# Optimization experiments

Hardware: AMD Instinct MI355X
Metric: run time of the kernel (lower is better)

The kernel has to match this reference:

```python
import jax, jax.numpy as jnp
import numpy as np

IN_C = 128
HIDE_C = 256
HC2 = HIDE_C // 2
OUT_C = 128
WS = 7          # winsize
SCALE = 0.125   # 1/8
EPS = 1e-5      # BatchNorm eps
B, H, W = 32, 112, 112


def setup_inputs() -> dict:
    key = jax.random.key(0)
    ks = jax.random.split(key, 24)
    f32 = jnp.float32

    def w(k, shape):
        return jax.random.normal(k, shape, f32) * 0.05

    def bn_params(k, c):
        k1, k2, k3, k4 = jax.random.split(k, 4)
        gamma = 1.0 + 0.1 * jax.random.normal(k1, (c,), f32)
        beta = 0.1 * jax.random.normal(k2, (c,), f32)
        mean = 0.1 * jax.random.normal(k3, (c,), f32)
        var = jax.random.uniform(k4, (c,), f32, 0.5, 1.5)
        return gamma, beta, mean, var

    x = jax.random.normal(ks[0], (B, IN_C, H, W), f32)
    wq = w(ks[1], (HC2, IN_C))
    gq, bq, mq, vq = bn_params(ks[2], HC2)
    wk = w(ks[3], (HC2, IN_C))
    gk, bk, mk, vk = bn_params(ks[4], HC2)
    wv = w(ks[5], (HIDE_C, IN_C))
    gv, bv, mv, vv = bn_params(ks[6], HIDE_C)
    wo = w(ks[7], (OUT_C, HIDE_C))
    bo = 0.05 * jax.random.normal(ks[8], (OUT_C,), f32)
    go, bbo, mo, vo = bn_params(ks[9], OUT_C)
    return {"x": x,
            "wq": wq, "gq": gq, "bq": bq, "mq": mq, "vq": vq,
            "wk": wk, "gk": gk, "bk": bk, "mk": mk, "vk": vk,
            "wv": wv, "gv": gv, "bv": bv, "mv": mv, "vv": vv,
            "wo": wo, "bo": bo, "go": go, "bbo": bbo, "mo": mo, "vo": vo}


def _conv1x1(x, w):
    # 1x1 conv, stride 1, no bias: pure channel contraction
    return jnp.einsum('bchw,oc->bohw', x, w)


def _bn(x, g, b, m, v):
    # inference-mode BatchNorm2d
    p = lambda a: a[None, :, None, None]
    return p(g) * (x - p(m)) * jax.lax.rsqrt(p(v) + EPS) + p(b)


def _to_windows(t):
    # 'b c (h1 ws1) (w1 ws2) -> b (c ws1 ws2) (h1 w1)'
    b, c, h, w = t.shape
    h1, w1 = h // WS, w // WS
    t = t.reshape(b, c, h1, WS, w1, WS).transpose(0, 1, 3, 5, 2, 4)
    return t.reshape(b, c * WS * WS, h1 * w1)


def _forward(x, wq, gq, bq, mq, vq, wk, gk, bk, mk, vk,
             wv, gv, bv, mv, vv, wo, bo, go, bbo, mo, vo):
    q = _bn(_conv1x1(x, wq), gq, bq, mq, vq)   # [B, HC2, H, W]
    k = _bn(_conv1x1(x, wk), gk, bk, mk, vk)   # [B, HC2, H, W]
    v = _bn(_conv1x1(x, wv), gv, bv, mv, vv)   # [B, HIDE_C, H, W]
    b, _, h, w = q.shape
    h1, w1 = h // WS, w // WS

    qf = _to_windows(q)  # [B, HC2*49, h1*w1]
    kf = _to_windows(k)
    vf = _to_windows(v)  # [B, HIDE_C*49, h1*w1]

    dots = jnp.einsum('bci,bcj->bij', qf, kf) * SCALE   # [B, T, T], T=h1*w1
    attn = jax.nn.softmax(dots, axis=-1)
    out = jnp.einsum('bij,bdj->bid', attn, vf)          # [B, T, HIDE_C*49]

    # 'b (h1 w1) (c1 ws1 ws2) -> b c1 (h1 ws1) (w1 ws2)'
    out = out.reshape(b, h1, w1, HIDE_C, WS, WS).transpose(0, 3, 1, 4, 2, 5)
    out = out.reshape(b, HIDE_C, h, w)

    out = jax.nn.gelu(out, approximate=False)
    out = _conv1x1(out, wo) + bo[None, :, None, None]
    out = _bn(out, go, bbo, mo, vo)
    # dropout is identity in eval; downsample is identity (stride=1, in_c==out_c)
    return jax.nn.gelu(out + x, approximate=False)


def reference(x, wq, gq, bq, mq, vq, wk, gk, bk, mk, vk,
              wv, gv, bv, mv, vv, wo, bo, go, bbo, mo, vo):
    return _forward(x, wq, gq, bq, mq, vq, wk, gk, bk, mk, vk,
                    wv, gv, bv, mv, vv, wo, bo, go, bbo, mo, vo)
```

## Files before the change

### kernel.cpp

```cpp
#include <hip/hip_runtime.h>


typedef unsigned short u16;
typedef unsigned int u32;
typedef short s16x8 __attribute__((ext_vector_type(8)));
typedef float f32x4 __attribute__((ext_vector_type(4)));
typedef u16 u16x8 __attribute__((ext_vector_type(8)));
typedef u16 u16x4 __attribute__((ext_vector_type(4)));

#define EPSV 1e-5f

__device__ __forceinline__ float bf2f(u16 h) {
  u32 u = ((u32)h) << 16;
  return __builtin_bit_cast(float, u);
}
__device__ __forceinline__ u16 f2bf(float f) {
  u32 u = __builtin_bit_cast(u32, f);
  u += 0x7FFFu + ((u >> 16) & 1u);
  return (u16)(u >> 16);
}
__device__ __forceinline__ s16x8 ld8(const u16* p) { return *(const s16x8*)p; }
__device__ __forceinline__ f32x4 mfma_bf16(s16x8 a, s16x8 b, f32x4 c) {
  return __builtin_amdgcn_mfma_f32_16x16x32_bf16(a, b, c, 0, 0, 0);
}
__device__ __forceinline__ float gelu_f(float v) {
  float e = exp2f(-2.3022083f * (v + 0.044715f * v * v * v));
  return v / (1.0f + e);
}

__global__ void k_params(
    const float* __restrict__ gq, const float* __restrict__ bq, const float* __restrict__ mq, const float* __restrict__ vq,
    const float* __restrict__ gk, const float* __restrict__ bk, const float* __restrict__ mk, const float* __restrict__ vk,
    const float* __restrict__ gv, const float* __restrict__ bv, const float* __restrict__ mv, const float* __restrict__ vv,
    const float* __restrict__ bo, const float* __restrict__ go, const float* __restrict__ bbo, const float* __restrict__ mo,
    const float* __restrict__ vo,
    float* __restrict__ sc512, float* __restrict__ sh512, float* __restrict__ sco, float* __restrict__ sho)
{
  const int i = threadIdx.x;
  if (i < 128) {
    const float s = gq[i] * rsqrtf(vq[i] + EPSV);
    sc512[i] = s;
    sh512[i] = bq[i] - mq[i] * s;
    const float so = go[i] * rsqrtf(vo[i] + EPSV);
    sco[i] = so;
    sho[i] = (bo[i] - mo[i]) * so + bbo[i];
  } else if (i < 256) {
    const int c = i - 128;
    const float s = gk[c] * rsqrtf(vk[c] + EPSV);
    sc512[i] = s;
    sh512[i] = bk[c] - mk[c] * s;
  } else if (i < 512) {
    const int c = i - 256;
    const float s = gv[c] * rsqrtf(vv[c] + EPSV);
    sc512[i] = s;
    sh512[i] = bv[c] - mv[c] * s;
  }
}

__global__ void k_wconv(const float* __restrict__ wq, const float* __restrict__ wk,
                        const float* __restrict__ wv, const float* __restrict__ sc512,
                        u16* __restrict__ wfused)
{
  const int idx4 = (blockIdx.x * 256 + threadIdx.x) * 4;
  const int co = idx4 >> 7, c = idx4 & 127;
  const float* src = (co < 128) ? (wq + co * 128 + c)
                   : (co < 256) ? (wk + (co - 128) * 128 + c)
                                : (wv + (co - 256) * 128 + c);
  const float s = sc512[co];
  const float4 v = *(const float4*)src;
  u16x4 r;
  r[0] = f2bf(v.x * s); r[1] = f2bf(v.y * s);
  r[2] = f2bf(v.z * s); r[3] = f2bf(v.w * s);
  *(u16x4*)(wfused + idx4) = r;
}

__global__ __launch_bounds__(256, 2) void k_qkv(
    const float* __restrict__ x, const u16* __restrict__ wfused,
    const float* __restrict__ sh512,
    u16* __restrict__ QW, u16* __restrict__ KW, u16* __restrict__ VW)
{
  __shared__ u16 XT[256 * 128];
  const int b = blockIdx.y;
  const int px0 = blockIdx.x * 256;
  const int t = threadIdx.x;

  {
    const float* xp = x + (size_t)b * 128u * 12544u + (size_t)(px0 + t);
    const int sw = (t & 15) << 3;
    #pragma unroll 8
    for (int c = 0; c < 128; c += 4) {
      u16x4 pk;
      pk[0] = f2bf(xp[(size_t)(c + 0) * 12544u]);
      pk[1] = f2bf(xp[(size_t)(c + 1) * 12544u]);
      pk[2] = f2bf(xp[(size_t)(c + 2) * 12544u]);
      pk[3] = f2bf(xp[(size_t)(c + 3) * 12544u]);
      *(u16x4*)&XT[t * 128 + (c ^ sw)] = pk;
    }
  }
  __syncthreads();

  const int w = t >> 6, l = t & 63, a15 = l & 15, g = l >> 4;

  s16x8 af[4][4];
  #pragma unroll
  for (int pxt = 0; pxt < 4; ++pxt) {
    const int row = w * 64 + pxt * 16 + a15;
    const int sw = (row & 15) << 3;
    #pragma unroll
    for (int ks = 0; ks < 4; ++ks) {
      const int cc = ks * 32 + g * 8;
      af[pxt][ks] = *(const s16x8*)&XT[row * 128 + (cc ^ sw)];
    }
  }
  __syncthreads();

  const int px = px0 + t;
  const int hh = px / 112, ww = px - hh * 112;
  const int h1 = hh / 7, p = hh - h1 * 7;
  const int w1 = ww / 7, q = ww - w1 * 7;
  const int j = h1 * 16 + w1, pq = p * 7 + q;
  u16* const qrow = QW + ((size_t)(b * 256 + j) * 49 + pq) * 128;
  u16* const krow = KW + ((size_t)(b * 256 + j) * 49 + pq) * 128;
  u16* const vrow = VW + (size_t)(b * 256 + j) * 12544 + pq * 256;

  #pragma unroll 1
  for (int phase = 0; phase < 4; ++phase) {
    s16x8 bcur[4];
    {
      const u16* wrow = wfused + (u32)(phase * 128 + a15) * 128u;
      #pragma unroll
      for (int ks = 0; ks < 4; ++ks) bcur[ks] = ld8(wrow + ks * 32 + g * 8);
    }
    #pragma unroll 1
    for (int cot8 = 0; cot8 < 8; ++cot8) {
      s16x8 bnext[4];
      if (cot8 < 7) {
        const u16* wrow = wfused + (u32)(phase * 128 + (cot8 + 1) * 16 + a15) * 128u;
        #pragma unroll
        for (int ks = 0; ks < 4; ++ks) bnext[ks] = ld8(wrow + ks * 32 + g * 8);
      }
      f32x4 acc[4];
      #pragma unroll
      for (int pxt = 0; pxt < 4; ++pxt) { acc[pxt][0]=0.f; acc[pxt][1]=0.f; acc[pxt][2]=0.f; acc[pxt][3]=0.f; }
      #pragma unroll
      for (int ks = 0; ks < 4; ++ks)
        #pragma unroll
        for (int pxt = 0; pxt < 4; ++pxt)
          acc[pxt] = mfma_bf16(af[pxt][ks], bcur[ks], acc[pxt]);

      const float sh = sh512[phase * 128 + cot8 * 16 + a15];
      const int co = cot8 * 16 + a15;
      #pragma unroll
      for (int pxt = 0; pxt < 4; ++pxt) {
        #pragma unroll
        for (int r = 0; r < 4; ++r) {
          const int pxl = w * 64 + pxt * 16 + g * 4 + r;
          XT[pxl * 128 + (co ^ ((pxl & 15) << 3))] = f2bf(acc[pxt][r] + sh);
        }
      }
      #pragma unroll
      for (int ks = 0; ks < 4; ++ks) bcur[ks] = bnext[ks];
    }
    __syncthreads();
    {
      u16* dst = (phase == 0) ? qrow : (phase == 1) ? krow : vrow + (phase - 2) * 128;
      const int sw = (t & 15) << 3;
      #pragma unroll
      for (int c8 = 0; c8 < 16; ++c8)
        *(u16x8*)(dst + c8 * 8) = *(const u16x8*)&XT[t * 128 + ((c8 * 8) ^ sw)];
    }
    __syncthreads();
  }
}

__global__ __launch_bounds__(512, 2) void k_dots(
    const u16* __restrict__ QW, const u16* __restrict__ KW, float* __restrict__ Pp)
{
  __shared__ u16 QS[256 * 64];
  __shared__ u16 KS[256 * 64];
  const int b = blockIdx.y, ks = blockIdx.x;
  const int nch = (ks == 7) ? 14 : 12;
  const int t = threadIdx.x;
  const int w = t >> 6, l = t & 63, a15 = l & 15, g = l >> 4;
  const int i0w = (w >> 1) * 64, j0w = (w & 1) * 128;

  f32x4 acc[4][8];
  #pragma unroll
  for (int i = 0; i < 4; ++i)
    #pragma unroll
    for (int j = 0; j < 8; ++j) { acc[i][j][0]=0.f; acc[i][j][1]=0.f; acc[i][j][2]=0.f; acc[i][j][3]=0.f; }

  const int srow = t >> 1;
  const int sgr0 = (t & 1) * 4;
  const size_t kb = (size_t)ks * 768 + (size_t)((t & 1) * 32);
  const u16* qsrc = QW + ((size_t)b * 256 + srow) * 6272 + kb;
  const u16* ksrc = KW + ((size_t)b * 256 + srow) * 6272 + kb;
  u16* qdst = &QS[srow * 64];
  u16* kdst = &KS[srow * 64];
  const int swr = srow & 7;

  for (int ch = 0; ch < nch; ++ch) {
    const int k0 = ch * 64;
    #pragma unroll
    for (int gi = 0; gi < 4; ++gi) {
      const int off = ((sgr0 + gi) ^ swr) << 3;
      *(u16x8*)(qdst + off) = *(const u16x8*)(qsrc + k0 + gi * 8);
      *(u16x8*)(kdst + off) = *(const u16x8*)(ksrc + k0 + gi * 8);
    }
    __syncthreads();
    #pragma unroll
    for (int kk = 0; kk < 2; ++kk) {
      s16x8 af[4], bfr[8];
      #pragma unroll
      for (int i4 = 0; i4 < 4; ++i4) {
        const int ir = i0w + i4 * 16 + a15;
        af[i4] = *(const s16x8*)&QS[ir * 64 + (((kk * 4 + g) ^ (ir & 7)) << 3)];
      }
      #pragma unroll
      for (int j8 = 0; j8 < 8; ++j8) {
        const int jr = j0w + j8 * 16 + a15;
        bfr[j8] = *(const s16x8*)&KS[jr * 64 + (((kk * 4 + g) ^ (jr & 7)) << 3)];
      }
      #pragma unroll
      for (int i4 = 0; i4 < 4; ++i4)
        #pragma unroll
        for (int j8 = 0; j8 < 8; ++j8)
          acc[i4][j8] = mfma_bf16(af[i4], bfr[j8], acc[i4][j8]);
    }
    __syncthreads();
  }

  float* pp = Pp + ((size_t)ks * 32 + b) * 256 * 256;
  #pragma unroll
  for (int i4 = 0; i4 < 4; ++i4)
    #pragma unroll
    for (int r = 0; r < 4; ++r) {
      const int ir = i0w + i4 * 16 + g * 4 + r;
      #pragma unroll
      for (int j8 = 0; j8 < 8; ++j8)
        pp[(size_t)ir * 256 + j0w + j8 * 16 + a15] = acc[i4][j8][r];
    }
}

__global__ __launch_bounds__(256, 4) void k_smax(const float* __restrict__ Pp, u16* __restrict__ P)
{
  const int b = blockIdx.y, it = blockIdx.x;
  const int t = threadIdx.x;
  const int row = it * 32 + (t >> 3);
  const int cg = t & 7;
  const size_t rb = ((size_t)b * 256 + row) * 256 + cg * 32;

  f32x4 s[8];
  #pragma unroll
  for (int cc = 0; cc < 8; ++cc) { s[cc][0]=0.f; s[cc][1]=0.f; s[cc][2]=0.f; s[cc][3]=0.f; }
  #pragma unroll 1
  for (int ks = 0; ks < 8; ++ks) {
    const float* src = Pp + (size_t)ks * 32 * 256 * 256 + rb;
    #pragma unroll
    for (int cc = 0; cc < 8; ++cc)
      s[cc] += *(const f32x4*)(src + cc * 4);
  }
  float m = -1e30f;
  #pragma unroll
  for (int cc = 0; cc < 8; ++cc)
    m = fmaxf(m, fmaxf(fmaxf(s[cc][0], s[cc][1]), fmaxf(s[cc][2], s[cc][3])));
  m = fmaxf(m, __shfl_xor(m, 1));
  m = fmaxf(m, __shfl_xor(m, 2));
  m = fmaxf(m, __shfl_xor(m, 4));
  const float CEXP = 0.18033688f;
  float sum = 0.f;
  #pragma unroll
  for (int cc = 0; cc < 8; ++cc)
    #pragma unroll
    for (int e = 0; e < 4; ++e) {
      const float p = exp2f((s[cc][e] - m) * CEXP);
      s[cc][e] = p;
      sum += p;
    }
  sum += __shfl_xor(sum, 1);
  sum += __shfl_xor(sum, 2);
  sum += __shfl_xor(sum, 4);
  const float inv = 1.0f / sum;
  u16* dst = P + rb;
  #pragma unroll
  for (int cc = 0; cc < 8; cc += 2) {
    u16x8 o;
    o[0] = f2bf(s[cc][0] * inv);     o[1] = f2bf(s[cc][1] * inv);
    o[2] = f2bf(s[cc][2] * inv);     o[3] = f2bf(s[cc][3] * inv);
    o[4] = f2bf(s[cc + 1][0] * inv); o[5] = f2bf(s[cc + 1][1] * inv);
    o[6] = f2bf(s[cc + 1][2] * inv); o[7] = f2bf(s[cc + 1][3] * inv);
    *(u16x8*)(dst + cc * 4) = o;
  }
}

__global__ __launch_bounds__(512, 2) void k_pv(
    const u16* __restrict__ P, const u16* __restrict__ VW, u16* __restrict__ GN)
{
  __shared__ u16 VT[256 * 64];
  __shared__ u16 PS[256 * 64];
  const int b = blockIdx.y, pq = blockIdx.x;
  const int t = threadIdx.x;
  const int w = t >> 6, l = t & 63, a15 = l & 15, g = l >> 4;
  const int m0w = (w >> 1) * 64, i0w = (w & 1) * 128;

  f32x4 acc[4][8];
  #pragma unroll
  for (int i = 0; i < 4; ++i)
    #pragma unroll
    for (int j = 0; j < 8; ++j) { acc[i][j][0]=0.f; acc[i][j][1]=0.f; acc[i][j][2]=0.f; acc[i][j][3]=0.f; }

  const int sj0 = (t & 7) * 8;
  const int sm0 = (t >> 3) * 4;
  const u16* vbase = VW + ((size_t)b * 256 + sj0) * 12544 + pq * 256 + sm0;
  const int prow = t >> 1;
  const int pgr0 = (t & 1) * 4;
  const u16* pbase = P + ((size_t)b * 256 + prow) * 256 + (t & 1) * 32;
  u16* psdst = &PS[prow * 64];
  const int pswr = prow & 7;

  for (int jc = 0; jc < 4; ++jc) {
    const int j0 = jc * 64;
    u16x4 rr[8];
    #pragma unroll
    for (int ji = 0; ji < 8; ++ji)
      rr[ji] = *(const u16x4*)(vbase + (size_t)(j0 + ji) * 12544);
    #pragma unroll
    for (int mi = 0; mi < 4; ++mi) {
      u16x8 wv;
      #pragma unroll
      for (int ji = 0; ji < 8; ++ji) wv[ji] = rr[ji][mi];
      const int m = sm0 + mi;
      *(u16x8*)&VT[m * 64 + (((sj0 >> 3) ^ (m & 7)) << 3)] = wv;
    }
    #pragma unroll
    for (int gi = 0; gi < 4; ++gi) {
      const int off = ((pgr0 + gi) ^ pswr) << 3;
      *(u16x8*)(psdst + off) = *(const u16x8*)(pbase + j0 + gi * 8);
    }
    __syncthreads();
    #pragma unroll
    for (int kk = 0; kk < 2; ++kk) {
      s16x8 av[4], bp[8];
      #pragma unroll
      for (int mf = 0; mf < 4; ++mf) {
        const int m = m0w + mf * 16 + a15;
        av[mf] = *(const s16x8*)&VT[m * 64 + (((kk * 4 + g) ^ (m & 7)) << 3)];
      }
      #pragma unroll
      for (int f = 0; f < 8; ++f) {
        const int i = i0w + f * 16 + a15;
        bp[f] = *(const s16x8*)&PS[i * 64 + (((kk * 4 + g) ^ (i & 7)) << 3)];
      }
      #pragma unroll
      for (int mf = 0; mf < 4; ++mf)
        #pragma unroll
        for (int f = 0; f < 8; ++f)
          acc[mf][f] = mfma_bf16(av[mf], bp[f], acc[mf][f]);
    }
    __syncthreads();
  }

  const int pp_ = pq / 7, qq = pq - 7 * pp_;
  #pragma unroll
  for (int f = 0; f < 8; ++f) {
    const int i = i0w + f * 16 + a15;
    const int h1 = i >> 4, w1 = i & 15;
    const size_t gb = ((size_t)b * 12544 + (size_t)((h1 * 7 + pp_) * 112 + w1 * 7 + qq)) * 256;
    #pragma unroll
    for (int mf = 0; mf < 4; ++mf) {
      u16x4 st;
      #pragma unroll
      for (int r = 0; r < 4; ++r) st[r] = f2bf(gelu_f(acc[mf][f][r]));
      *(u16x4*)&GN[gb + m0w + mf * 16 + g * 4] = st;
    }
  }
}

__global__ __launch_bounds__(512, 2) void k_out(
    const u16* __restrict__ GN, const float* __restrict__ wo,
    const float* __restrict__ x, const float* __restrict__ sco,
    const float* __restrict__ sho, float* __restrict__ out)
{
  __shared__ u16 WO[128 * 256];
  __shared__ u16 OT[128 * 264];
  const int b = blockIdx.y;
  const int px0 = blockIdx.x * 256;
  const int t = threadIdx.x;
  const int w = t >> 6, l = t & 63, a15 = l & 15, g = l >> 4;

  {
    const int o = t >> 2, gr0 = (t & 3) * 8;
    const float s = sco[o];
    const float* src = wo + o * 256 + gr0 * 8;
    u16* dr = &WO[o * 256];
    #pragma unroll
    for (int gi = 0; gi < 8; ++gi) {
      const float4 v0 = *(const float4*)(src + gi * 8);
      const float4 v1 = *(const float4*)(src + gi * 8 + 4);
      u16x8 pk;
      pk[0] = f2bf(v0.x * s); pk[1] = f2bf(v0.y * s);
      pk[2] = f2bf(v0.z * s); pk[3] = f2bf(v0.w * s);
      pk[4] = f2bf(v1.x * s); pk[5] = f2bf(v1.y * s);
      pk[6] = f2bf(v1.z * s); pk[7] = f2bf(v1.w * s);
      *(u16x8*)(dr + (((gr0 + gi) ^ (o & 7)) << 3)) = pk;
    }
  }
  __syncthreads();

  const int pw = w >> 1, ow = w & 1;
  const int o0w = ow * 64;
  f32x4 acc[4][4];
  #pragma unroll
  for (int i = 0; i < 4; ++i)
    #pragma unroll
    for (int j = 0; j < 4; ++j) { acc[i][j][0]=0.f; acc[i][j][1]=0.f; acc[i][j][2]=0.f; acc[i][j][3]=0.f; }

  #pragma unroll 1
  for (int ksl = 0; ksl < 8; ++ksl) {
    s16x8 af[4], bw[4];
    #pragma unroll
    for (int pxf = 0; pxf < 4; ++pxf) {
      const int row = px0 + pw * 64 + pxf * 16 + a15;
      af[pxf] = ld8(GN + ((size_t)b * 12544 + row) * 256 + ksl * 32 + g * 8);
    }
    #pragma unroll
    for (int of = 0; of < 4; ++of) {
      const int o = o0w + of * 16 + a15;
      bw[of] = *(const s16x8*)&WO[o * 256 + (((ksl * 4 + g) ^ (o & 7)) << 3)];
    }
    #pragma unroll
    for (int pxf = 0; pxf < 4; ++pxf)
      #pragma unroll
      for (int of = 0; of < 4; ++of)
        acc[pxf][of] = mfma_bf16(af[pxf], bw[of], acc[pxf][of]);
  }

  #pragma unroll
  for (int pxf = 0; pxf < 4; ++pxf)
    #pragma unroll
    for (int of = 0; of < 4; ++of) {
      u16x4 st;
      #pragma unroll
      for (int r = 0; r < 4; ++r) st[r] = f2bf(acc[pxf][of][r]);
      *(u16x4*)&OT[(o0w + of * 16 + a15) * 264 + pw * 64 + pxf * 16 + g * 4] = st;
    }
  __syncthreads();

  const int o2 = t >> 2;
  const float sh = sho[o2];
  const size_t xb = ((size_t)b * 128 + o2) * 12544 + px0;
  #pragma unroll 2
  for (int ii = 0; ii < 16; ++ii) {
    const int po = ii * 16 + (t & 3) * 4;
    const u16x4 zt = *(const u16x4*)&OT[o2 * 264 + po];
    const float4 xv = *(const float4*)(x + xb + po);
    float4 r;
    r.x = gelu_f(bf2f(zt[0]) + sh + xv.x);
    r.y = gelu_f(bf2f(zt[1]) + sh + xv.y);
    r.z = gelu_f(bf2f(zt[2]) + sh + xv.z);
    r.w = gelu_f(bf2f(zt[3]) + sh + xv.w);
    *(float4*)(out + xb + po) = r;
  }
}

extern "C" void kernel_launch(void* const* d_in, const int* in_sizes, int n_in,
                              void* d_out, int out_size, void* d_ws, size_t ws_size,
                              hipStream_t stream) {
  (void)in_sizes; (void)n_in; (void)out_size; (void)ws_size;
  const float* x   = (const float*)d_in[0];
  const float* wq  = (const float*)d_in[1];
  const float* gq  = (const float*)d_in[2];
  const float* bq  = (const float*)d_in[3];
  const float* mq  = (const float*)d_in[4];
  const float* vq  = (const float*)d_in[5];
  const float* wk  = (const float*)d_in[6];
  const float* gk  = (const float*)d_in[7];
  const float* bk  = (const float*)d_in[8];
  const float* mk  = (const float*)d_in[9];
  const float* vk  = (const float*)d_in[10];
  const float* wv  = (const float*)d_in[11];
  const float* gv  = (const float*)d_in[12];
  const float* bv  = (const float*)d_in[13];
  const float* mv  = (const float*)d_in[14];
  const float* vv  = (const float*)d_in[15];
  const float* wo  = (const float*)d_in[16];
  const float* bo  = (const float*)d_in[17];
  const float* go  = (const float*)d_in[18];
  const float* bbo = (const float*)d_in[19];
  const float* mo  = (const float*)d_in[20];
  const float* vo  = (const float*)d_in[21];

  u16* QW = (u16*)d_ws;
  u16* KW = QW + 51380224u;
  u16* VW = KW + 51380224u;
  u16* GN = VW + 102760448u;
  u16* P  = QW;
  float* Pp = (float*)GN;
  u16* wfused = GN;
  float* sc512 = (float*)(GN + 102760448u);
  float* sh512 = sc512 + 512;
  float* sco = sh512 + 512;
  float* sho = sco + 128;

  k_params<<<1, 512, 0, stream>>>(gq, bq, mq, vq, gk, bk, mk, vk, gv, bv, mv, vv,
                                  bo, go, bbo, mo, vo, sc512, sh512, sco, sho);
  k_wconv<<<64, 256, 0, stream>>>(wq, wk, wv, sc512, wfused);
  k_qkv<<<dim3(49, 32), 256, 0, stream>>>(x, wfused, sh512, QW, KW, VW);
  k_dots<<<dim3(8, 32), 512, 0, stream>>>(QW, KW, Pp);
  k_smax<<<dim3(8, 32), 256, 0, stream>>>(Pp, P);
  k_pv<<<dim3(49, 32), 512, 0, stream>>>(P, VW, GN);
  k_out<<<dim3(49, 32), 512, 0, stream>>>(GN, wo, x, sco, sho, (float*)d_out);
}
```

Baseline: 743.0 us.

## Precompute scaled bf16 output weights and retile qkv/out kernels for occupancy

Output-projection weights are now scaled and converted to bf16 once by a new kernel, in a workspace slot freed after the dots stage. The out kernel no longer stages them in LDS on every block and instead reads them from global/L2, using half-size pixel tiles with 256 threads to raise occupancy. k_qkv moves to 512 threads per block, with each wave handling 32 pixels and each thread half the channels, again to raise occupancy. The cost is extra global weight loads and one more kernel launch, and wof reuses KW memory, which relies on KW being dead by then.

```diff
diff --git a/kernel.cpp b/kernel.cpp
--- a/kernel.cpp
+++ b/kernel.cpp
@@ -74,7 +74,20 @@
   *(u16x4*)(wfused + idx4) = r;
 }
 
-__global__ __launch_bounds__(256, 2) void k_qkv(
+__global__ void k_woconv(const float* __restrict__ wo, const float* __restrict__ sco,
+                         u16* __restrict__ wof)
+{
+  const int idx4 = (blockIdx.x * 256 + threadIdx.x) * 4;
+  const int o = idx4 >> 8;
+  const float s = sco[o];
+  const float4 v = *(const float4*)(wo + idx4);
+  u16x4 r;
+  r[0] = f2bf(v.x * s); r[1] = f2bf(v.y * s);
+  r[2] = f2bf(v.z * s); r[3] = f2bf(v.w * s);
+  *(u16x4*)(wof + idx4) = r;
+}
+
+__global__ __launch_bounds__(512, 4) void k_qkv(
     const float* __restrict__ x, const u16* __restrict__ wfused,
     const float* __restrict__ sh512,
     u16* __restrict__ QW, u16* __restrict__ KW, u16* __restrict__ VW)
@@ -85,43 +98,45 @@
   const int t = threadIdx.x;
 
   {
-    const float* xp = x + (size_t)b * 128u * 12544u + (size_t)(px0 + t);
-    const int sw = (t & 15) << 3;
-    #pragma unroll 8
-    for (int c = 0; c < 128; c += 4) {
+    const int pxl = t & 255, cb = (t >> 8) * 64;
+    const float* xp = x + (size_t)b * 128u * 12544u + (size_t)cb * 12544u + (size_t)(px0 + pxl);
+    const int sw = (pxl & 15) << 3;
+    #pragma unroll 4
+    for (int i = 0; i < 16; ++i) {
+      const int c = i * 4;
       u16x4 pk;
       pk[0] = f2bf(xp[(size_t)(c + 0) * 12544u]);
       pk[1] = f2bf(xp[(size_t)(c + 1) * 12544u]);
       pk[2] = f2bf(xp[(size_t)(c + 2) * 12544u]);
       pk[3] = f2bf(xp[(size_t)(c + 3) * 12544u]);
-      *(u16x4*)&XT[t * 128 + (c ^ sw)] = pk;
+      *(u16x4*)&XT[pxl * 128 + ((cb + c) ^ sw)] = pk;
     }
   }
   __syncthreads();
 
   const int w = t >> 6, l = t & 63, a15 = l & 15, g = l >> 4;
 
-  s16x8 af[4][4];
-  #pragma unroll
-  for (int pxt = 0; pxt < 4; ++pxt) {
-    const int row = w * 64 + pxt * 16 + a15;
+  s16x8 af[2][4];
+  #pragma unroll
+  for (int pxt = 0; pxt < 2; ++pxt) {
+    const int row = w * 32 + pxt * 16 + a15;
     const int sw = (row & 15) << 3;
     #pragma unroll
-    for (int ks = 0; ks < 4; ++ks) {
-      const int cc = ks * 32 + g * 8;
-      af[pxt][ks] = *(const s16x8*)&XT[row * 128 + (cc ^ sw)];
-    }
+    for (int ks = 0; ks < 4; ++ks)
+      af[pxt][ks] = *(const s16x8*)&XT[row * 128 + ((ks * 32 + g * 8) ^ sw)];
   }
   __syncthreads();
 
-  const int px = px0 + t;
+  const int pxl = t & 255, chalf = (t >> 8) * 64;
+  const int px = px0 + pxl;
   const int hh = px / 112, ww = px - hh * 112;
   const int h1 = hh / 7, p = hh - h1 * 7;
   const int w1 = ww / 7, q = ww - w1 * 7;
   const int j = h1 * 16 + w1, pq = p * 7 + q;
-  u16* const qrow = QW + ((size_t)(b * 256 + j) * 49 + pq) * 128;
-  u16* const krow = KW + ((size_t)(b * 256 + j) * 49 + pq) * 128;
-  u16* const vrow = VW + (size_t)(b * 256 + j) * 12544 + pq * 256;
+  u16* const qrow = QW + ((size_t)(b * 256 + j) * 49 + pq) * 128 + chalf;
+  u16* const krow = KW + ((size_t)(b * 256 + j) * 49 + pq) * 128 + chalf;
+  u16* const vrow = VW + (size_t)(b * 256 + j) * 12544 + pq * 256 + chalf;
+  const int swf = (pxl & 15) << 3;
 
   #pragma unroll 1
   for (int phase = 0; phase < 4; ++phase) {
@@ -139,23 +154,23 @@
         #pragma unroll
         for (int ks = 0; ks < 4; ++ks) bnext[ks] = ld8(wrow + ks * 32 + g * 8);
       }
-      f32x4 acc[4];
-      #pragma unroll
-      for (int pxt = 0; pxt < 4; ++pxt) { acc[pxt][0]=0.f; acc[pxt][1]=0.f; acc[pxt][2]=0.f; acc[pxt][3]=0.f; }
+      f32x4 acc[2];
+      #pragma unroll
+      for (int pxt = 0; pxt < 2; ++pxt) { acc[pxt][0]=0.f; acc[pxt][1]=0.f; acc[pxt][2]=0.f; acc[pxt][3]=0.f; }
       #pragma unroll
       for (int ks = 0; ks < 4; ++ks)
         #pragma unroll
-        for (int pxt = 0; pxt < 4; ++pxt)
+        for (int pxt = 0; pxt < 2; ++pxt)
           acc[pxt] = mfma_bf16(af[pxt][ks], bcur[ks], acc[pxt]);
 
       const float sh = sh512[phase * 128 + cot8 * 16 + a15];
       const int co = cot8 * 16 + a15;
       #pragma unroll
-      for (int pxt = 0; pxt < 4; ++pxt) {
+      for (int pxt = 0; pxt < 2; ++pxt) {
         #pragma unroll
         for (int r = 0; r < 4; ++r) {
-          const int pxl = w * 64 + pxt * 16 + g * 4 + r;
-          XT[pxl * 128 + (co ^ ((pxl & 15) << 3))] = f2bf(acc[pxt][r] + sh);
+          const int prow = w * 32 + pxt * 16 + g * 4 + r;
+          XT[prow * 128 + (co ^ ((prow & 15) << 3))] = f2bf(acc[pxt][r] + sh);
         }
       }
       #pragma unroll
@@ -164,10 +179,9 @@
     __syncthreads();
     {
       u16* dst = (phase == 0) ? qrow : (phase == 1) ? krow : vrow + (phase - 2) * 128;
-      const int sw = (t & 15) << 3;
-      #pragma unroll
-      for (int c8 = 0; c8 < 16; ++c8)
-        *(u16x8*)(dst + c8 * 8) = *(const u16x8*)&XT[t * 128 + ((c8 * 8) ^ sw)];
+      #pragma unroll
+      for (int c8 = 0; c8 < 8; ++c8)
+        *(u16x8*)(dst + c8 * 8) = *(const u16x8*)&XT[pxl * 128 + ((chalf + c8 * 8) ^ swf)];
     }
     __syncthreads();
   }
@@ -376,39 +390,17 @@
   }
 }
 
-__global__ __launch_bounds__(512, 2) void k_out(
-    const u16* __restrict__ GN, const float* __restrict__ wo,
-    const float* __restrict__ x, const float* __restrict__ sco,
-    const float* __restrict__ sho, float* __restrict__ out)
-{
-  __shared__ u16 WO[128 * 256];
-  __shared__ u16 OT[128 * 264];
+__global__ __launch_bounds__(256, 3) void k_out(
+    const u16* __restrict__ GN, const u16* __restrict__ wof,
+    const float* __restrict__ x, const float* __restrict__ sho, float* __restrict__ out)
+{
+  __shared__ u16 OT[128 * 140];
   const int b = blockIdx.y;
-  const int px0 = blockIdx.x * 256;
+  const int px0 = blockIdx.x * 128;
   const int t = threadIdx.x;
   const int w = t >> 6, l = t & 63, a15 = l & 15, g = l >> 4;
-
-  {
-    const int o = t >> 2, gr0 = (t & 3) * 8;
-    const float s = sco[o];
-    const float* src = wo + o * 256 + gr0 * 8;
-    u16* dr = &WO[o * 256];
-    #pragma unroll
-    for (int gi = 0; gi < 8; ++gi) {
-      const float4 v0 = *(const float4*)(src + gi * 8);
-      const float4 v1 = *(const float4*)(src + gi * 8 + 4);
-      u16x8 pk;
-      pk[0] = f2bf(v0.x * s); pk[1] = f2bf(v0.y * s);
-      pk[2] = f2bf(v0.z * s); pk[3] = f2bf(v0.w * s);
-      pk[4] = f2bf(v1.x * s); pk[5] = f2bf(v1.y * s);
-      pk[6] = f2bf(v1.z * s); pk[7] = f2bf(v1.w * s);
-      *(u16x8*)(dr + (((gr0 + gi) ^ (o & 7)) << 3)) = pk;
-    }
-  }
-  __syncthreads();
-
   const int pw = w >> 1, ow = w & 1;
-  const int o0w = ow * 64;
+
   f32x4 acc[4][4];
   #pragma unroll
   for (int i = 0; i < 4; ++i)
@@ -425,8 +417,8 @@
     }
     #pragma unroll
     for (int of = 0; of < 4; ++of) {
-      const int o = o0w + of * 16 + a15;
-      bw[of] = *(const s16x8*)&WO[o * 256 + (((ksl * 4 + g) ^ (o & 7)) << 3)];
+      const int o = ow * 64 + of * 16 + a15;
+      bw[of] = ld8(wof + (u32)o * 256u + (u32)(ksl * 32 + g * 8));
     }
     #pragma unroll
     for (int pxf = 0; pxf < 4; ++pxf)
@@ -442,24 +434,24 @@
       u16x4 st;
       #pragma unroll
       for (int r = 0; r < 4; ++r) st[r] = f2bf(acc[pxf][of][r]);
-      *(u16x4*)&OT[(o0w + of * 16 + a15) * 264 + pw * 64 + pxf * 16 + g * 4] = st;
+      *(u16x4*)&OT[(ow * 64 + of * 16 + a15) * 140 + pw * 64 + pxf * 16 + g * 4] = st;
     }
   __syncthreads();
 
-  const int o2 = t >> 2;
-  const float sh = sho[o2];
-  const size_t xb = ((size_t)b * 128 + o2) * 12544 + px0;
-  #pragma unroll 2
+  const int o = t >> 1;
+  const int half = (t & 1) * 64;
+  const float sh = sho[o];
+  const size_t xb = ((size_t)b * 128 + o) * 12544 + px0 + half;
+  #pragma unroll 4
   for (int ii = 0; ii < 16; ++ii) {
-    const int po = ii * 16 + (t & 3) * 4;
-    const u16x4 zt = *(const u16x4*)&OT[o2 * 264 + po];
-    const float4 xv = *(const float4*)(x + xb + po);
+    const u16x4 zt = *(const u16x4*)&OT[o * 140 + half + ii * 4];
+    const float4 xv = *(const float4*)(x + xb + ii * 4);
     float4 r;
     r.x = gelu_f(bf2f(zt[0]) + sh + xv.x);
     r.y = gelu_f(bf2f(zt[1]) + sh + xv.y);
     r.z = gelu_f(bf2f(zt[2]) + sh + xv.z);
     r.w = gelu_f(bf2f(zt[3]) + sh + xv.w);
-    *(float4*)(out + xb + po) = r;
+    *(float4*)(out + xb + ii * 4) = r;
   }
 }
 
@@ -495,6 +487,7 @@
   u16* VW = KW + 51380224u;
   u16* GN = VW + 102760448u;
   u16* P  = QW;
+  u16* wof = KW;
   float* Pp = (float*)GN;
   u16* wfused = GN;
   float* sc512 = (float*)(GN + 102760448u);
@@ -505,9 +498,10 @@
   k_params<<<1, 512, 0, stream>>>(gq, bq, mq, vq, gk, bk, mk, vk, gv, bv, mv, vv,
                                   bo, go, bbo, mo, vo, sc512, sh512, sco, sho);
   k_wconv<<<64, 256, 0, stream>>>(wq, wk, wv, sc512, wfused);
-  k_qkv<<<dim3(49, 32), 256, 0, stream>>>(x, wfused, sh512, QW, KW, VW);
+  k_qkv<<<dim3(49, 32), 512, 0, stream>>>(x, wfused, sh512, QW, KW, VW);
   k_dots<<<dim3(8, 32), 512, 0, stream>>>(QW, KW, Pp);
   k_smax<<<dim3(8, 32), 256, 0, stream>>>(Pp, P);
+  k_woconv<<<32, 256, 0, stream>>>(wo, sco, wof);
   k_pv<<<dim3(49, 32), 512, 0, stream>>>(P, VW, GN);
-  k_out<<<dim3(49, 32), 512, 0, stream>>>(GN, wo, x, sco, sho, (float*)d_out);
-}
+  k_out<<<dim3(98, 32), 256, 0, stream>>>(GN, wof, x, sho, (float*)d_out);
+}
```

Measured after the change: 876.4 us. +18.0%, slower.
